# Kernel tuning notes

Measured on AMD Instinct MI355X. Metric: run time of the kernel, lower is better.

## Reference

```python
import jax, jax.numpy as jnp
import numpy as np

B, C, T = 128, 295, 2048
D1 = 270
NUM_SUBJECTS = 64

def setup_inputs() -> dict:
    key = jax.random.key(0)
    k_x, k_s, k_w1, k_b1, k_ws = jax.random.split(key, 5)
    X = jax.random.normal(k_x, (B, C, T), dtype=jnp.float32)
    subject_idxs = jax.random.randint(k_s, (B,), 0, NUM_SUBJECTS)
    W1 = jax.random.normal(k_w1, (D1, C), dtype=jnp.float32) * 0.05
    b1 = jax.random.normal(k_b1, (D1,), dtype=jnp.float32) * 0.05
    Ws = jax.random.normal(k_ws, (NUM_SUBJECTS, D1, D1), dtype=jnp.float32) * 0.05
    return {"X": X, "subject_idxs": subject_idxs, "W1": W1, "b1": b1, "Ws": Ws}

def reference(X, subject_idxs, W1, b1, Ws):
    # Shared 1x1 conv: pointwise channel mix C -> D1 with bias.  [B, D1, T]
    y = jnp.einsum('dc,bct->bdt', W1, X) + b1[None, :, None]
    # Top-1 expert dispatch: gather each sample's subject matrix. [B, D1, D1]
    W_sel = Ws[subject_idxs]
    # Per-sample 1x1 conv (batched GEMM), no bias.            [B, D1, T]
    out = jnp.einsum('bed,bdt->bet', W_sel, y)
    return out
```

## Files before the change

kernel.cpp:

```cpp
#include <hip/hip_runtime.h>

#define NSUBJ 64
#define CIN   295
#define DD    270
#define TT    2048
#define BB    128

#define WF_PER_S  92160
#define WF_PER_KS 9216
#define W1T_PER_KS 10240

typedef __attribute__((ext_vector_type(8))) short bf16x8;
typedef __attribute__((ext_vector_type(4))) float f32x4;
typedef unsigned short u16;

__device__ __forceinline__ u16 f2bf(float f) {
    union { float f; unsigned int u; } v; v.f = f;
    unsigned int r = v.u + 0x7FFFu + ((v.u >> 16) & 1u);
    return (u16)(r >> 16);
}

__device__ __forceinline__ void glds16(const u16* g, u16* lds_base) {
    __builtin_amdgcn_global_load_lds(
        (const __attribute__((address_space(1))) unsigned int*)g,
        (__attribute__((address_space(3))) unsigned int*)lds_base, 16, 0, 0);
}

#define WAITV(N) asm volatile("s_waitcnt vmcnt(" #N ")" ::: "memory")
#define WAITL()  asm volatile("s_waitcnt lgkmcnt(0)" ::: "memory")
#define BAR()    __builtin_amdgcn_s_barrier()
#define SB()     __builtin_amdgcn_sched_barrier(0)

__global__ __launch_bounds__(256) void k_prep_w1(const float* __restrict__ W1,
                                                 const float* __restrict__ b1,
                                                 u16* __restrict__ W1t)
{
    const int idx = blockIdx.x * 256 + threadIdx.x;
    const int ks = idx / W1T_PER_KS;
    const int r  = idx - ks * W1T_PER_KS;
    const int kq = r / 2560;
    const int c  = (r - kq * 2560) >> 3;
    const int k8 = r & 7;
    const int d  = ks * 32 + kq * 8 + k8;
    float v = 0.f;
    if (d < DD) {
        if (c < CIN) v = W1[d * CIN + c];
        else if (c == CIN) v = b1[d];
    }
    W1t[idx] = f2bf(v);
}

__global__ __launch_bounds__(256, 1) void k_fuse_w(const float* __restrict__ Ws,
                                                   const u16* __restrict__ W1t,
                                                   u16* __restrict__ Wf)
{
    __shared__ u16 Aw[3072];
    __shared__ u16 Bw[10240];
    const int tid = threadIdx.x, lane = tid & 63, wid = tid >> 6;
    const int wm = wid >> 1, wn = wid & 1;
    const int mt = blockIdx.x, s = blockIdx.y;
    const int e0 = mt * 96;
    const float* Wsb = Ws + (size_t)s * DD * DD;

    f32x4 acc[3][10];
#pragma unroll
    for (int i = 0; i < 3; ++i)
#pragma unroll
        for (int j = 0; j < 10; ++j) acc[i][j] = (f32x4){0.f, 0.f, 0.f, 0.f};

    for (int ks = 0; ks < 9; ++ks) {
        const int k0 = ks * 32;
#pragma unroll
        for (int ci = 0; ci < 3; ++ci) {
            const int id = tid + ci * 256;
            const int m = id >> 3, q = id & 7;
            const int e = e0 + m, d = k0 + q * 4;
            float2 v01 = {0.f, 0.f}, v23 = {0.f, 0.f};
            if (e < DD) {
                if (d < DD)     v01 = *(const float2*)(Wsb + (size_t)e * DD + d);
                if (d + 2 < DD) v23 = *(const float2*)(Wsb + (size_t)e * DD + d + 2);
            }
            ushort4 h;
            h.x = f2bf(v01.x); h.y = f2bf(v01.y); h.z = f2bf(v23.x); h.w = f2bf(v23.y);
            *(ushort4*)(&Aw[(q >> 1) * 768 + m * 8 + (q & 1) * 4]) = h;
        }
#pragma unroll
        for (int k5 = 0; k5 < 5; ++k5) {
            const int seg = wid * 5 + k5;
            glds16(W1t + (size_t)ks * W1T_PER_KS + seg * 512 + lane * 8, &Bw[seg * 512]);
        }
        __syncthreads();
        bf16x8 af[3];
#pragma unroll
        for (int i = 0; i < 3; ++i)
            af[i] = *(const bf16x8*)(&Aw[(lane >> 4) * 768 + (wm * 48 + i * 16 + (lane & 15)) * 8]);
#pragma unroll
        for (int j = 0; j < 10; ++j) {
            const bf16x8 bfj = *(const bf16x8*)(&Bw[(lane >> 4) * 2560 + (wn * 160 + j * 16 + (lane & 15)) * 8]);
#pragma unroll
            for (int i = 0; i < 3; ++i)
                acc[i][j] = __builtin_amdgcn_mfma_f32_16x16x32_bf16(af[i], bfj, acc[i][j], 0, 0, 0);
        }
        __syncthreads();
    }
    const int rb = (lane >> 4) * 4, cc = lane & 15;
#pragma unroll
    for (int i = 0; i < 3; ++i) {
#pragma unroll
        for (int r = 0; r < 4; ++r) {
            const int e = e0 + wm * 48 + i * 16 + rb + r;
#pragma unroll
            for (int j = 0; j < 10; ++j) {
                const int c = wn * 160 + j * 16 + cc;
                Wf[(size_t)s * WF_PER_S + (c >> 5) * WF_PER_KS + ((c >> 3) & 3) * 2304
                   + e * 8 + (c & 7)] = f2bf(acc[i][j][r]);
            }
        }
    }
}

__global__ __launch_bounds__(256, 2) void k_main(const float* __restrict__ X,
                                                 const int* __restrict__ subj,
                                                 const u16* __restrict__ Wf,
                                                 float* __restrict__ out)
{
    __shared__ u16 Am[2][9216];
    __shared__ u16 Bm[2][2048];
    const int tid = threadIdx.x, lane = tid & 63, wid = tid >> 6;
    const int wm = wid >> 1, wn = wid & 1;
    const int nt = blockIdx.x, b = blockIdx.y;
    const int t0 = nt * 64;
    const int s = subj[b];
    const float* Xb = X + (size_t)b * CIN * TT;
    const u16* WfA = Wf + (size_t)s * WF_PER_S;
    const int bn = tid & 63, bkq = tid >> 6;

    f32x4 acc[9][2];
#pragma unroll
    for (int i = 0; i < 9; ++i)
#pragma unroll
        for (int j = 0; j < 2; ++j) acc[i][j] = (f32x4){0.f, 0.f, 0.f, 0.f};

    float xrE[8], xrO[8];

#define LOADB(KS, XR, CL)                                                   \
    {                                                                       \
        _Pragma("unroll")                                                   \
        for (int q = 0; q < 8; ++q) {                                       \
            const int c = (KS) * 32 + bkq * 8 + q;                          \
            const int cl = ((CL) && c >= CIN) ? (c - 33) : c;               \
            XR[q] = Xb[(size_t)cl * TT + t0 + bn];                          \
        }                                                                   \
    }
#define WRITEB(KS, XR)                                                      \
    {                                                                       \
        bf16x8 h;                                                           \
        _Pragma("unroll")                                                   \
        for (int q = 0; q < 8; ++q) {                                       \
            const int c = (KS) * 32 + bkq * 8 + q;                          \
            u16 v = f2bf(XR[q]);                                            \
            if (c >= CIN) v = (c == CIN) ? (u16)0x3F80 : (u16)0;            \
            h[q] = (short)v;                                                \
        }                                                                   \
        *(bf16x8*)(&Bm[(KS) & 1][bkq * 512 + bn * 8]) = h;                  \
    }
#define STAGEA(KS)                                                          \
    {                                                                       \
        _Pragma("unroll")                                                   \
        for (int k5 = 0; k5 < 5; ++k5) {                                    \
            int seg = wid * 5 + k5;                                         \
            if (seg >= 18) seg -= 18;                                       \
            glds16(WfA + (size_t)(KS) * WF_PER_KS + seg * 512 + lane * 8,   \
                   &Am[(KS) & 1][seg * 512]);                               \
        }                                                                   \
    }
#define COMPUTE(CUR)                                                        \
    {                                                                       \
        bf16x8 bfr[2];                                                      \
        _Pragma("unroll")                                                   \
        for (int j = 0; j < 2; ++j)                                         \
            bfr[j] = *(const bf16x8*)(&Bm[CUR][(lane >> 4) * 512 + (wn * 32 + j * 16 + (lane & 15)) * 8]); \
        _Pragma("unroll")                                                   \
        for (int i = 0; i < 9; ++i) {                                       \
            const bf16x8 af = *(const bf16x8*)(&Am[CUR][(lane >> 4) * 2304 + (wm * 144 + i * 16 + (lane & 15)) * 8]); \
            acc[i][0] = __builtin_amdgcn_mfma_f32_16x16x32_bf16(af, bfr[0], acc[i][0], 0, 0, 0); \
            acc[i][1] = __builtin_amdgcn_mfma_f32_16x16x32_bf16(af, bfr[1], acc[i][1], 0, 0, 0); \
        }                                                                   \
    }

    LOADB(0, xrE, 0); SB();
    STAGEA(0);        SB();
    LOADB(1, xrO, 0); SB();
    WAITV(13);
    WRITEB(0, xrE);
    WAITV(8);
    WAITL(); BAR();

#define STEP(KS, XLD, XWR, CL)                                              \
    {                                                                       \
        STAGEA((KS) + 1);        SB();                                      \
        LOADB((KS) + 2, XLD, CL); SB();                                     \
        COMPUTE((KS) & 1);                                                  \
        WAITV(13);                                     \
        WRITEB((KS) + 1, XWR);                                              \
        WAITV(8);                   \
        WAITL(); BAR();                                                     \
    }
    for (int kk = 0; kk < 3; ++kk) {
        STEP(2 * kk,     xrE, xrO, 0);
        STEP(2 * kk + 1, xrO, xrE, 0);
    }
    STEP(6, xrE, xrO, 0);
    STEP(7, xrO, xrE, 1);
    STAGEA(9); SB();
    COMPUTE(0);
    WAITV(5);
    WRITEB(9, xrO);
    WAITV(0); WAITL(); BAR();
    COMPUTE(1);

    const int rb = (lane >> 4) * 4, cc = lane & 15;
#pragma unroll
    for (int i = 0; i < 9; ++i) {
#pragma unroll
        for (int r = 0; r < 4; ++r) {
            const int e = wm * 144 + i * 16 + rb + r;
            if (e < DD) {
#pragma unroll
                for (int j = 0; j < 2; ++j) {
                    const int t = t0 + wn * 32 + j * 16 + cc;
                    out[((size_t)b * DD + e) * TT + t] = acc[i][j][r];
                }
            }
        }
    }
#undef LOADB
#undef WRITEB
#undef STAGEA
#undef COMPUTE
#undef STEP
}

extern "C" void kernel_launch(void* const* d_in, const int* in_sizes, int n_in,
                              void* d_out, int out_size, void* d_ws, size_t ws_size,
                              hipStream_t stream) {
    const float* X    = (const float*)d_in[0];
    const int*   subj = (const int*)d_in[1];
    const float* W1   = (const float*)d_in[2];
    const float* b1   = (const float*)d_in[3];
    const float* Ws   = (const float*)d_in[4];
    float* out = (float*)d_out;

    u16* Wf  = (u16*)d_ws;
    u16* W1t = (u16*)((char*)d_ws + (size_t)NSUBJ * WF_PER_S * 2);

    k_prep_w1<<<dim3(360), 256, 0, stream>>>(W1, b1, W1t);
    k_fuse_w<<<dim3(3, NSUBJ), 256, 0, stream>>>(Ws, W1t, Wf);
    k_main<<<dim3(TT / 64, BB), 256, 0, stream>>>(X, subj, Wf, out);
}
```

Measured before the change: 194.7 us.

## Widen main GEMM tile to 128 time columns with 512-thread blocks and swizzled grid

The main kernel now uses 512 threads (8 wavefronts in a 2x4 layout) covering 128 time steps per block instead of 64. Each staged tile of fused weights in LDS is therefore reused across twice as many columns, which halves the weight traffic per output. Only the first six wavefronts stage weights, three segments each, and the wait counts are adjusted to match. The grid is flattened and remapped so that consecutive blocks spread across batches and time tiles, aiming for better cache locality. This raises LDS use per block and changes occupancy, and the mixed staging roles add divergent control flow around the barriers.

```diff
diff --git a/kernel.cpp b/kernel.cpp
--- a/kernel.cpp
+++ b/kernel.cpp
@@ -119,21 +119,24 @@
     }
 }
 
-__global__ __launch_bounds__(256, 2) void k_main(const float* __restrict__ X,
+__global__ __launch_bounds__(512, 4) void k_main(const float* __restrict__ X,
                                                  const int* __restrict__ subj,
                                                  const u16* __restrict__ Wf,
                                                  float* __restrict__ out)
 {
     __shared__ u16 Am[2][9216];
-    __shared__ u16 Bm[2][2048];
+    __shared__ u16 Bm[2][4096];
     const int tid = threadIdx.x, lane = tid & 63, wid = tid >> 6;
-    const int wm = wid >> 1, wn = wid & 1;
-    const int nt = blockIdx.x, b = blockIdx.y;
-    const int t0 = nt * 64;
+    const int wm = wid >> 2, wn = wid & 3;
+    const int hw = blockIdx.x;
+    const int w  = (hw & 7) * 256 + (hw >> 3);
+    const int b  = w >> 4, nt = w & 15;
+    const int t0 = nt * 128;
     const int s = subj[b];
     const float* Xb = X + (size_t)b * CIN * TT;
     const u16* WfA = Wf + (size_t)s * WF_PER_S;
-    const int bn = tid & 63, bkq = tid >> 6;
+    const int bn = tid & 127, bkq = tid >> 7;
+    const bool stg = (wid < 6);
 
     f32x4 acc[9][2];
 #pragma unroll
@@ -162,14 +165,13 @@
             if (c >= CIN) v = (c == CIN) ? (u16)0x3F80 : (u16)0;            \
             h[q] = (short)v;                                                \
         }                                                                   \
-        *(bf16x8*)(&Bm[(KS) & 1][bkq * 512 + bn * 8]) = h;                  \
+        *(bf16x8*)(&Bm[(KS) & 1][bkq * 1024 + bn * 8]) = h;                 \
     }
 #define STAGEA(KS)                                                          \
     {                                                                       \
         _Pragma("unroll")                                                   \
-        for (int k5 = 0; k5 < 5; ++k5) {                                    \
-            int seg = wid * 5 + k5;                                         \
-            if (seg >= 18) seg -= 18;                                       \
+        for (int k3 = 0; k3 < 3; ++k3) {                                    \
+            const int seg = wid * 3 + k3;                                   \
             glds16(WfA + (size_t)(KS) * WF_PER_KS + seg * 512 + lane * 8,   \
                    &Am[(KS) & 1][seg * 512]);                               \
         }                                                                   \
@@ -179,7 +181,7 @@
         bf16x8 bfr[2];                                                      \
         _Pragma("unroll")                                                   \
         for (int j = 0; j < 2; ++j)                                         \
-            bfr[j] = *(const bf16x8*)(&Bm[CUR][(lane >> 4) * 512 + (wn * 32 + j * 16 + (lane & 15)) * 8]); \
+            bfr[j] = *(const bf16x8*)(&Bm[CUR][(lane >> 4) * 1024 + (wn * 32 + j * 16 + (lane & 15)) * 8]); \
         _Pragma("unroll")                                                   \
         for (int i = 0; i < 9; ++i) {                                       \
             const bf16x8 af = *(const bf16x8*)(&Am[CUR][(lane >> 4) * 2304 + (wm * 144 + i * 16 + (lane & 15)) * 8]); \
@@ -188,35 +190,58 @@
         }                                                                   \
     }
 
-    LOADB(0, xrE, 0); SB();
-    STAGEA(0);        SB();
-    LOADB(1, xrO, 0); SB();
-    WAITV(13);
-    WRITEB(0, xrE);
-    WAITV(8);
-    WAITL(); BAR();
+    if (stg) {
+        LOADB(0, xrE, 0); SB();
+        STAGEA(0);        SB();
+        LOADB(1, xrO, 0); SB();
+        WAITV(11);
+        WRITEB(0, xrE);
+        WAITV(8);
+        WAITL();
+    } else {
+        LOADB(0, xrE, 0); SB();
+        LOADB(1, xrO, 0); SB();
+        WAITV(8);
+        WRITEB(0, xrE);
+        WAITL();
+    }
+    BAR();
 
 #define STEP(KS, XLD, XWR, CL)                                              \
-    {                                                                       \
-        STAGEA((KS) + 1);        SB();                                      \
+    if (stg) {                                                              \
+        STAGEA((KS) + 1);         SB();                                     \
         LOADB((KS) + 2, XLD, CL); SB();                                     \
         COMPUTE((KS) & 1);                                                  \
-        WAITV(13);                                     \
+        WAITV(11);                                     \
         WRITEB((KS) + 1, XWR);                                              \
+        WAITV(8);                \
+        WAITL();                                                            \
+        BAR();                                                              \
+    } else {                                                                \
+        LOADB((KS) + 2, XLD, CL); SB();                                     \
+        COMPUTE((KS) & 1);                                                  \
         WAITV(8);                   \
-        WAITL(); BAR();                                                     \
-    }
-    for (int kk = 0; kk < 3; ++kk) {
+        WRITEB((KS) + 1, XWR);                                              \
+        WAITL();                                                            \
+        BAR();                                                              \
+    }
+    for (int kk = 0; kk < 4; ++kk) {
         STEP(2 * kk,     xrE, xrO, 0);
-        STEP(2 * kk + 1, xrO, xrE, 0);
-    }
-    STEP(6, xrE, xrO, 0);
-    STEP(7, xrO, xrE, 1);
-    STAGEA(9); SB();
-    COMPUTE(0);
-    WAITV(5);
-    WRITEB(9, xrO);
-    WAITV(0); WAITL(); BAR();
+        STEP(2 * kk + 1, xrO, xrE, (2 * kk + 1 == 7));
+    }
+    if (stg) {
+        STAGEA(9); SB();
+        COMPUTE(0);
+        WAITV(3);
+        WRITEB(9, xrO);
+        WAITV(0); WAITL();
+    } else {
+        COMPUTE(0);
+        WAITV(0);
+        WRITEB(9, xrO);
+        WAITL();
+    }
+    BAR();
     COMPUTE(1);
 
     const int rb = (lane >> 4) * 4, cc = lane & 15;
@@ -256,5 +281,5 @@
 
     k_prep_w1<<<dim3(360), 256, 0, stream>>>(W1, b1, W1t);
     k_fuse_w<<<dim3(3, NSUBJ), 256, 0, stream>>>(Ws, W1t, Wf);
-    k_main<<<dim3(TT / 64, BB), 256, 0, stream>>>(X, subj, Wf, out);
-}
+    k_main<<<dim3(TT / 128 * BB), 512, 0, stream>>>(X, subj, Wf, out);
+}
```

Result: slower. 709.6 us (+264.5%).

## Stage X tiles via direct global-to-LDS loads as fp32, convert to bf16 at fragment read

Applied to the files above, without the earlier changes.

X is now copied into LDS in fp32 with global_load_lds and an XOR swizzle, replacing the register loads, in-register bf16 conversion and LDS stores. Conversion to bf16 and the bias/padding row handling move into the MFMA fragment-building step. The hand-tuned waitcnt/sched_barrier pipeline is replaced by a simple unrolled double-buffer loop using __syncthreads, and A staging drops its redundant duplicate segment loads. The cost is a larger fp32 X buffer in LDS, eight scalar LDS reads plus conversions per fragment, and less explicit control over load latency hiding.

```diff
diff --git a/kernel.cpp b/kernel.cpp
--- a/kernel.cpp
+++ b/kernel.cpp
@@ -1,4 +1,5 @@
 #include <hip/hip_runtime.h>
+#include <hip/hip_bf16.h>
 
 #define NSUBJ 64
 #define CIN   295
@@ -15,21 +16,14 @@
 typedef unsigned short u16;
 
 __device__ __forceinline__ u16 f2bf(float f) {
-    union { float f; unsigned int u; } v; v.f = f;
-    unsigned int r = v.u + 0x7FFFu + ((v.u >> 16) & 1u);
-    return (u16)(r >> 16);
-}
-
-__device__ __forceinline__ void glds16(const u16* g, u16* lds_base) {
+    return __bfloat16_as_ushort(__float2bfloat16(f));
+}
+
+__device__ __forceinline__ void glds16(const void* g, void* lds_base) {
     __builtin_amdgcn_global_load_lds(
         (const __attribute__((address_space(1))) unsigned int*)g,
         (__attribute__((address_space(3))) unsigned int*)lds_base, 16, 0, 0);
 }
-
-#define WAITV(N) asm volatile("s_waitcnt vmcnt(" #N ")" ::: "memory")
-#define WAITL()  asm volatile("s_waitcnt lgkmcnt(0)" ::: "memory")
-#define BAR()    __builtin_amdgcn_s_barrier()
-#define SB()     __builtin_amdgcn_sched_barrier(0)
 
 __global__ __launch_bounds__(256) void k_prep_w1(const float* __restrict__ W1,
                                                  const float* __restrict__ b1,
@@ -124,8 +118,8 @@
                                                  const u16* __restrict__ Wf,
                                                  float* __restrict__ out)
 {
-    __shared__ u16 Am[2][9216];
-    __shared__ u16 Bm[2][2048];
+    __shared__ u16   Am[2][9216];
+    __shared__ float Xm[2][2048];
     const int tid = threadIdx.x, lane = tid & 63, wid = tid >> 6;
     const int wm = wid >> 1, wn = wid & 1;
     const int nt = blockIdx.x, b = blockIdx.y;
@@ -133,7 +127,7 @@
     const int s = subj[b];
     const float* Xb = X + (size_t)b * CIN * TT;
     const u16* WfA = Wf + (size_t)s * WF_PER_S;
-    const int bn = tid & 63, bkq = tid >> 6;
+    const int g = lane >> 4;
 
     f32x4 acc[9][2];
 #pragma unroll
@@ -141,85 +135,66 @@
 #pragma unroll
         for (int j = 0; j < 2; ++j) acc[i][j] = (f32x4){0.f, 0.f, 0.f, 0.f};
 
-    float xrE[8], xrO[8];
-
-#define LOADB(KS, XR, CL)                                                   \
-    {                                                                       \
-        _Pragma("unroll")                                                   \
-        for (int q = 0; q < 8; ++q) {                                       \
-            const int c = (KS) * 32 + bkq * 8 + q;                          \
-            const int cl = ((CL) && c >= CIN) ? (c - 33) : c;               \
-            XR[q] = Xb[(size_t)cl * TT + t0 + bn];                          \
-        }                                                                   \
-    }
-#define WRITEB(KS, XR)                                                      \
-    {                                                                       \
-        bf16x8 h;                                                           \
-        _Pragma("unroll")                                                   \
-        for (int q = 0; q < 8; ++q) {                                       \
-            const int c = (KS) * 32 + bkq * 8 + q;                          \
-            u16 v = f2bf(XR[q]);                                            \
-            if (c >= CIN) v = (c == CIN) ? (u16)0x3F80 : (u16)0;            \
-            h[q] = (short)v;                                                \
-        }                                                                   \
-        *(bf16x8*)(&Bm[(KS) & 1][bkq * 512 + bn * 8]) = h;                  \
-    }
 #define STAGEA(KS)                                                          \
     {                                                                       \
         _Pragma("unroll")                                                   \
         for (int k5 = 0; k5 < 5; ++k5) {                                    \
-            int seg = wid * 5 + k5;                                         \
-            if (seg >= 18) seg -= 18;                                       \
-            glds16(WfA + (size_t)(KS) * WF_PER_KS + seg * 512 + lane * 8,   \
-                   &Am[(KS) & 1][seg * 512]);                               \
-        }                                                                   \
-    }
-#define COMPUTE(CUR)                                                        \
+            const int seg = wid + 4 * k5;                                   \
+            if (seg < 18)                                                   \
+                glds16(WfA + (size_t)(KS) * WF_PER_KS + seg * 512 + lane * 8,\
+                       &Am[(KS) & 1][seg * 512]);                           \
+        }                                                                   \
+    }
+#define STAGEX(KS)                                                          \
     {                                                                       \
+        _Pragma("unroll")                                                   \
+        for (int k2 = 0; k2 < 2; ++k2) {                                    \
+            const int seg = wid * 2 + k2;                                   \
+            const int cr0 = (KS) * 32 + seg * 4 + g;                        \
+            const int cr  = (cr0 < CIN) ? cr0 : (CIN - 1);                  \
+            const int sc  = (lane & 15) ^ (((seg >> 1) & 3) << 2);          \
+            glds16(Xb + (size_t)cr * TT + t0 + sc * 4,                      \
+                   &Xm[(KS) & 1][seg * 256]);                               \
+        }                                                                   \
+    }
+#define COMPUTE(KS, LAST)                                                   \
+    {                                                                       \
+        const float* Xc = &Xm[(KS) & 1][0];                                 \
         bf16x8 bfr[2];                                                      \
         _Pragma("unroll")                                                   \
-        for (int j = 0; j < 2; ++j)                                         \
-            bfr[j] = *(const bf16x8*)(&Bm[CUR][(lane >> 4) * 512 + (wn * 32 + j * 16 + (lane & 15)) * 8]); \
+        for (int j = 0; j < 2; ++j) {                                       \
+            const int tsw = (wn * 32 + j * 16 + (lane & 15)) ^ (g << 4);    \
+            bf16x8 bb;                                                      \
+            _Pragma("unroll")                                               \
+            for (int q = 0; q < 8; ++q) {                                   \
+                float v = Xc[(g * 8 + q) * 64 + tsw];                       \
+                if (LAST) {                                                 \
+                    if (q == 7)      v = (g == 0) ? 1.0f : 0.0f;            \
+                    else if (g > 0)  v = 0.0f;                              \
+                }                                                           \
+                bb[q] = (short)f2bf(v);                                     \
+            }                                                               \
+            bfr[j] = bb;                                                    \
+        }                                                                   \
         _Pragma("unroll")                                                   \
         for (int i = 0; i < 9; ++i) {                                       \
-            const bf16x8 af = *(const bf16x8*)(&Am[CUR][(lane >> 4) * 2304 + (wm * 144 + i * 16 + (lane & 15)) * 8]); \
+            const bf16x8 af = *(const bf16x8*)(&Am[(KS) & 1][g * 2304 + (wm * 144 + i * 16 + (lane & 15)) * 8]); \
             acc[i][0] = __builtin_amdgcn_mfma_f32_16x16x32_bf16(af, bfr[0], acc[i][0], 0, 0, 0); \
             acc[i][1] = __builtin_amdgcn_mfma_f32_16x16x32_bf16(af, bfr[1], acc[i][1], 0, 0, 0); \
         }                                                                   \
     }
 
-    LOADB(0, xrE, 0); SB();
-    STAGEA(0);        SB();
-    LOADB(1, xrO, 0); SB();
-    WAITV(13);
-    WRITEB(0, xrE);
-    WAITV(8);
-    WAITL(); BAR();
-
-#define STEP(KS, XLD, XWR, CL)                                              \
-    {                                                                       \
-        STAGEA((KS) + 1);        SB();                                      \
-        LOADB((KS) + 2, XLD, CL); SB();                                     \
-        COMPUTE((KS) & 1);                                                  \
-        WAITV(13);                                     \
-        WRITEB((KS) + 1, XWR);                                              \
-        WAITV(8);                   \
-        WAITL(); BAR();                                                     \
-    }
-    for (int kk = 0; kk < 3; ++kk) {
-        STEP(2 * kk,     xrE, xrO, 0);
-        STEP(2 * kk + 1, xrO, xrE, 0);
-    }
-    STEP(6, xrE, xrO, 0);
-    STEP(7, xrO, xrE, 1);
-    STAGEA(9); SB();
-    COMPUTE(0);
-    WAITV(5);
-    WRITEB(9, xrO);
-    WAITV(0); WAITL(); BAR();
-    COMPUTE(1);
-
-    const int rb = (lane >> 4) * 4, cc = lane & 15;
+    STAGEA(0); STAGEX(0);
+    __syncthreads();
+
+#pragma unroll
+    for (int ks = 0; ks < 10; ++ks) {
+        if (ks < 9) { STAGEA(ks + 1); STAGEX(ks + 1); }
+        COMPUTE(ks, (ks == 9));
+        __syncthreads();
+    }
+
+    const int rb = g * 4, cc = lane & 15;
 #pragma unroll
     for (int i = 0; i < 9; ++i) {
 #pragma unroll
@@ -234,11 +209,9 @@
             }
         }
     }
-#undef LOADB
-#undef WRITEB
 #undef STAGEA
+#undef STAGEX
 #undef COMPUTE
-#undef STEP
 }
 
 extern "C" void kernel_launch(void* const* d_in, const int* in_sizes, int n_in,
```

Result: no change. 192.5 us (-1.1%).
